# Kernel optimization log

Measured on AMD Instinct MI355X. Metric: run time of the kernel, lower is better.

The kernel has to match this reference:

```python
import jax, jax.numpy as jnp
from jax import lax
import numpy as np

B = 16
E, NH, FF, L = 768, 12, 3072, 8
D = E // NH  # 64, per-head dim
PATCH_DIM = 16 * 16 * 16  # 4096


def setup_inputs() -> dict:
    key = jax.random.key(0)
    ks = jax.random.split(key, 16)
    s = 0.02
    def n(k, shape):
        return jax.random.normal(k, shape, dtype=jnp.float32) * s
    return {
        "x": jax.random.normal(ks[0], (B, 512, 512, 3), dtype=jnp.float32),
        "conv1_w": n(ks[1], (3, 3, 3, 16)), "conv1_b": jnp.zeros((16,), jnp.float32),
        "conv2_w": n(ks[2], (3, 3, 16, 16)), "conv2_b": jnp.zeros((16,), jnp.float32),
        "proj_w": n(ks[3], (PATCH_DIM, E)), "proj_b": jnp.zeros((E,), jnp.float32),
        "Wq": n(ks[4], (L, E, E)), "bq": jnp.zeros((L, E), jnp.float32),
        "Wk": n(ks[5], (L, E, E)), "bk": jnp.zeros((L, E), jnp.float32),
        "Wv": n(ks[6], (L, E, E)), "bv": jnp.zeros((L, E), jnp.float32),
        "Wo": n(ks[7], (L, E, E)), "bo": jnp.zeros((L, E), jnp.float32),
        "W1": n(ks[8], (L, E, FF)), "b1": jnp.zeros((L, FF), jnp.float32),
        "W2": n(ks[9], (L, FF, E)), "b2": jnp.zeros((L, E), jnp.float32),
        "ln1_g": jnp.ones((L, E), jnp.float32), "ln1_b": jnp.zeros((L, E), jnp.float32),
        "ln2_g": jnp.ones((L, E), jnp.float32), "ln2_b": jnp.zeros((L, E), jnp.float32),
        "head_w": n(ks[10], (E, 1)), "head_b": jnp.zeros((1,), jnp.float32),
    }


def _ln(x, g, b, eps=1e-6):
    m = jnp.mean(x, axis=-1, keepdims=True)
    v = jnp.var(x, axis=-1, keepdims=True)
    return (x - m) * lax.rsqrt(v + eps) * g + b


def _forward(x, conv1_w, conv1_b, conv2_w, conv2_b, proj_w, proj_b,
             Wq, bq, Wk, bk, Wv, bv, Wo, bo, W1, b1, W2, b2,
             ln1_g, ln1_b, ln2_g, ln2_b, head_w, head_b):
    dn = ('NHWC', 'HWIO', 'NHWC')
    h = jax.nn.relu(lax.conv_general_dilated(x, conv1_w, (1, 1), 'VALID', dimension_numbers=dn) + conv1_b)
    h = lax.reduce_window(h, -jnp.inf, lax.max, (1, 2, 2, 1), (1, 2, 2, 1), 'VALID')  # (B,255,255,16)
    h = jax.nn.relu(lax.conv_general_dilated(h, conv2_w, (1, 1), 'VALID', dimension_numbers=dn) + conv2_b)
    h = lax.reduce_window(h, -jnp.inf, lax.max, (1, 2, 2, 1), (1, 2, 2, 1), 'VALID')  # (B,126,126,16)
    # tf.image.extract_patches 16x16 stride 16 SAME: pad 126 -> 128 (1 before, 1 after)
    h = jnp.pad(h, ((0, 0), (1, 1), (1, 1), (0, 0)))
    Bc = h.shape[0]
    patches = h.reshape(Bc, 8, 16, 8, 16, 16).transpose(0, 1, 3, 2, 4, 5).reshape(Bc, 64, PATCH_DIM)
    t = patches @ proj_w + proj_b  # (B,64,768)
    scale = 1.0 / jnp.sqrt(jnp.float32(D))  # tf code scales by sqrt(per-head key dim)
    for i in range(L):
        q = (t @ Wq[i] + bq[i]).reshape(Bc, -1, NH, D).transpose(0, 2, 1, 3)
        k = (t @ Wk[i] + bk[i]).reshape(Bc, -1, NH, D).transpose(0, 2, 1, 3)
        v = (t @ Wv[i] + bv[i]).reshape(Bc, -1, NH, D).transpose(0, 2, 1, 3)
        w = jax.nn.softmax(jnp.einsum('bhqd,bhkd->bhqk', q, k) * scale, axis=-1)
        a = jnp.einsum('bhqk,bhkd->bhqd', w, v)  # (B,H,S,D)
        # FAITHFUL to original: reshape (B,H,S,D) -> (B,S,E) directly (no transpose back)
        a = a.reshape(Bc, -1, E)
        a = a @ Wo[i] + bo[i]
        o1 = _ln(t + a, ln1_g[i], ln1_b[i])
        f = jax.nn.relu(o1 @ W1[i] + b1[i]) @ W2[i] + b2[i]
        t = _ln(o1 + f, ln2_g[i], ln2_b[i])
    pooled = jnp.mean(t, axis=1)  # GlobalAveragePooling1D
    return jax.nn.sigmoid(pooled @ head_w + head_b)


def reference(x, conv1_w, conv1_b, conv2_w, conv2_b, proj_w, proj_b,
              Wq, bq, Wk, bk, Wv, bv, Wo, bo, W1, b1, W2, b2,
              ln1_g, ln1_b, ln2_g, ln2_b, head_w, head_b):
    return _forward(x, conv1_w, conv1_b, conv2_w, conv2_b, proj_w, proj_b,
                    Wq, bq, Wk, bk, Wv, bv, Wo, bo, W1, b1, W2, b2,
                    ln1_g, ln1_b, ln2_g, ln2_b, head_w, head_b)
```

## Files before the change

### kernel.cpp

```cpp
#include <hip/hip_runtime.h>
#include <hip/hip_bf16.h>
#include <cstdint>
#include <cstddef>

typedef __bf16 bf16;
typedef __attribute__((ext_vector_type(8))) __bf16 bf16x8;
typedef __attribute__((ext_vector_type(4))) float f32x4;

__global__ __launch_bounds__(256) void wtrans(const float* __restrict__ src,
    bf16* __restrict__ dst, int K, int N) {
  __shared__ float tile[32][33];
  int l = blockIdx.z;
  src += (size_t)l * K * N; dst += (size_t)l * K * N;
  int n0 = blockIdx.x * 32, k0 = blockIdx.y * 32;
  int tx = threadIdx.x & 31, ty = threadIdx.x >> 5;
#pragma unroll
  for (int i = 0; i < 4; i++) {
    int k = ty + i * 8;
    tile[k][tx] = src[(size_t)(k0 + k) * N + n0 + tx];
  }
  __syncthreads();
#pragma unroll
  for (int i = 0; i < 4; i++) {
    int n = ty + i * 8;
    dst[(size_t)(n0 + n) * K + k0 + tx] = (bf16)tile[tx][n];
  }
}

__global__ __launch_bounds__(256) void conv1_mfma(const float* __restrict__ x,
    const float* __restrict__ w, const float* __restrict__ bias,
    bf16* __restrict__ out) {
  __shared__ alignas(16) bf16 xs[34 * 35 * 8];
  int t = threadIdx.x;
  int bx = blockIdx.x, by = blockIdx.y, b = blockIdx.z;
  int r0 = 32 * by, c0 = 32 * bx;
  for (int i = t; i < 34 * 35; i += 256) {
    int rr = i / 35, cc = i % 35;
    int gr = min(r0 + rr, 511), gc = min(c0 + cc, 511);
    const float* ip = x + ((size_t)(b * 512 + gr) * 512 + gc) * 3;
    bf16x8 pv = {(bf16)ip[0], (bf16)ip[1], (bf16)ip[2],
                 (bf16)0.f, (bf16)0.f, (bf16)0.f, (bf16)0.f, (bf16)0.f};
    *(bf16x8*)&xs[i * 8] = pv;
  }
  int lane = t & 63, wave = t >> 6;
  int lr = lane & 15, lq = lane >> 4;
  bf16x8 bfrag[3];
#pragma unroll
  for (int ky = 0; ky < 3; ky++) {
    bf16x8 v;
#pragma unroll
    for (int j = 0; j < 8; j++)
      v[j] = (lq < 3 && j < 3) ? (bf16)w[((ky * 3 + lq) * 3 + j) * 16 + lr] : (bf16)0.f;
    bfrag[ky] = v;
  }
  float bco = bias[lr];
  __syncthreads();
#pragma unroll
  for (int yy = 0; yy < 4; yy++) {
    int Y = wave * 4 + yy;
    int yp = by * 16 + Y;
    int cy = 2 * Y;
#pragma unroll
    for (int hx = 0; hx < 2; hx++) {
      f32x4 a0 = {0.f, 0.f, 0.f, 0.f}, a1 = {0.f, 0.f, 0.f, 0.f};
      int pbase = hx * 16 + lr + lq;
#pragma unroll
      for (int ky = 0; ky < 3; ky++) {
        bf16x8 f0 = *(const bf16x8*)&xs[((cy + ky) * 35 + pbase) * 8];
        a0 = __builtin_amdgcn_mfma_f32_16x16x32_bf16(f0, bfrag[ky], a0, 0, 0, 0);
      }
#pragma unroll
      for (int ky = 0; ky < 3; ky++) {
        bf16x8 f1 = *(const bf16x8*)&xs[((cy + 1 + ky) * 35 + pbase) * 8];
        a1 = __builtin_amdgcn_mfma_f32_16x16x32_bf16(f1, bfrag[ky], a1, 0, 0, 0);
      }
      float m0 = fmaxf(fmaxf(a0[0], a0[1]), fmaxf(a1[0], a1[1]));
      float m1 = fmaxf(fmaxf(a0[2], a0[3]), fmaxf(a1[2], a1[3]));
      m0 = fmaxf(m0 + bco, 0.f);
      m1 = fmaxf(m1 + bco, 0.f);
      int xp0 = bx * 16 + hx * 8 + 2 * lq, xp1 = xp0 + 1;
      if (yp < 255) {
        bf16* op = out + ((size_t)(b * 255 + yp) * 255) * 16 + lr;
        if (xp0 < 255) op[xp0 * 16] = (bf16)m0;
        if (xp1 < 255) op[xp1 * 16] = (bf16)m1;
      }
    }
  }
}

__global__ __launch_bounds__(256) void conv2_mfma(const bf16* __restrict__ in,
    const float* __restrict__ w, const float* __restrict__ bias,
    bf16* __restrict__ patches) {
  __shared__ alignas(16) bf16 xlo[1156 * 8];
  __shared__ alignas(16) bf16 xhi[1156 * 8];
  __shared__ float ws[2304];
  int t = threadIdx.x;
  int tx = blockIdx.x, ty = blockIdx.y, b = blockIdx.z;
  for (int i = t; i < 2304; i += 256) ws[i] = w[i];
  int r0 = 32 * ty - 2, c0 = 32 * tx - 2;
  for (int i = t; i < 1156; i += 256) {
    int rr = i / 34, cc = i % 34;
    int gr = min(max(r0 + rr, 0), 254), gc = min(max(c0 + cc, 0), 254);
    const bf16* ip = in + ((size_t)(b * 255 + gr) * 255 + gc) * 16;
    *(uint4*)&xlo[i * 8] = *(const uint4*)ip;
    *(uint4*)&xhi[i * 8] = *(const uint4*)(ip + 8);
  }
  __syncthreads();
  int lane = t & 63, wave = t >> 6;
  int lr = lane & 15, lq = lane >> 4;
  int tapsel = lq >> 1;
  int ci0 = (lq & 1) * 8;
  bf16x8 bfrag[5];
  int koff[5];
#pragma unroll
  for (int c2 = 0; c2 < 5; c2++) {
    int tap = 2 * c2 + tapsel;
    bf16x8 v;
#pragma unroll
    for (int j = 0; j < 8; j++)
      v[j] = (tap < 9) ? (bf16)ws[tap * 256 + (ci0 + j) * 16 + lr] : (bf16)0.f;
    bfrag[c2] = v;
    int tc = min(tap, 8);
    koff[c2] = (tc / 3) * 34 + (tc % 3);
  }
  const bf16* plane = (lq & 1) ? xhi : xlo;
  float bco = bias[lr];
  bf16* pout = patches + ((size_t)(b * 64 + ty * 8 + tx) * 4096);
#pragma unroll
  for (int yy = 0; yy < 4; yy++) {
    int Y = wave * 4 + yy;
    int yp = ty * 16 + Y;
    bool padrow = (yp == 0 || yp == 127);
#pragma unroll
    for (int hx = 0; hx < 2; hx++) {
      f32x4 a0 = {0.f, 0.f, 0.f, 0.f}, a1 = {0.f, 0.f, 0.f, 0.f};
      int base0 = (2 * Y) * 34 + hx * 16 + lr;
      int base1 = base0 + 34;
#pragma unroll
      for (int c2 = 0; c2 < 5; c2++) {
        bf16x8 f0 = *(const bf16x8*)&plane[(base0 + koff[c2]) * 8];
        a0 = __builtin_amdgcn_mfma_f32_16x16x32_bf16(f0, bfrag[c2], a0, 0, 0, 0);
      }
#pragma unroll
      for (int c2 = 0; c2 < 5; c2++) {
        bf16x8 f1 = *(const bf16x8*)&plane[(base1 + koff[c2]) * 8];
        a1 = __builtin_amdgcn_mfma_f32_16x16x32_bf16(f1, bfrag[c2], a1, 0, 0, 0);
      }
      float m0 = fmaxf(fmaxf(a0[0], a0[1]), fmaxf(a1[0], a1[1]));
      float m1 = fmaxf(fmaxf(a0[2], a0[3]), fmaxf(a1[2], a1[3]));
      m0 = fmaxf(m0 + bco, 0.f);
      m1 = fmaxf(m1 + bco, 0.f);
      int px0 = hx * 8 + 2 * lq, px1 = px0 + 1;
      int xp0 = tx * 16 + px0, xp1 = xp0 + 1;
      if (padrow || xp0 == 0) m0 = 0.f;
      if (padrow || xp1 == 127) m1 = 0.f;
      pout[Y * 256 + px0 * 16 + lr] = (bf16)m0;
      pout[Y * 256 + px1 * 16 + lr] = (bf16)m1;
    }
  }
}

#define LSTR 72

template<int MODE>
__device__ __forceinline__ void gemm_core(const bf16* __restrict__ A,
    const bf16* __restrict__ Bt, const float* __restrict__ bias,
    float* __restrict__ Cf, bf16* __restrict__ Cb,
    int bm, int bn, int N, int K, int k0, int kc) {
  __shared__ alignas(16) bf16 As[64 * LSTR];
  __shared__ alignas(16) bf16 Bs[64 * LSTR];
  int t = threadIdx.x, lane = t & 63, wave = t >> 6;
  int wm = (wave >> 1) * 32, wn = (wave & 1) * 32;
  int lq = lane >> 4, lr = lane & 15;
  f32x4 acc[2][2];
#pragma unroll
  for (int i = 0; i < 2; i++)
#pragma unroll
  for (int j = 0; j < 2; j++) acc[i][j] = (f32x4){0.f, 0.f, 0.f, 0.f};
  int r = t >> 2, c = (t & 3) * 16;
  const bf16* Ap = A + (size_t)(bm + r) * K + k0 + c;
  const bf16* Bp = Bt + (size_t)(bn + r) * K + k0 + c;
  bf16* AsW = &As[r * LSTR + c];
  bf16* BsW = &Bs[r * LSTR + c];
  uint4 a0 = *(const uint4*)Ap, a1 = *(const uint4*)(Ap + 8);
  uint4 b0 = *(const uint4*)Bp, b1 = *(const uint4*)(Bp + 8);
  for (int kk = 64; kk <= kc; kk += 64) {
    *(uint4*)AsW = a0; *(uint4*)(AsW + 8) = a1;
    *(uint4*)BsW = b0; *(uint4*)(BsW + 8) = b1;
    __syncthreads();
    if (kk < kc) {
      Ap += 64; Bp += 64;
      a0 = *(const uint4*)Ap; a1 = *(const uint4*)(Ap + 8);
      b0 = *(const uint4*)Bp; b1 = *(const uint4*)(Bp + 8);
    }
#pragma unroll
    for (int ks = 0; ks < 2; ks++) {
      bf16x8 af0 = *(const bf16x8*)&As[(wm + lr) * LSTR + ks * 32 + lq * 8];
      bf16x8 af1 = *(const bf16x8*)&As[(wm + 16 + lr) * LSTR + ks * 32 + lq * 8];
      bf16x8 bfr0 = *(const bf16x8*)&Bs[(wn + lr) * LSTR + ks * 32 + lq * 8];
      bf16x8 bfr1 = *(const bf16x8*)&Bs[(wn + 16 + lr) * LSTR + ks * 32 + lq * 8];
      acc[0][0] = __builtin_amdgcn_mfma_f32_16x16x32_bf16(af0, bfr0, acc[0][0], 0, 0, 0);
      acc[0][1] = __builtin_amdgcn_mfma_f32_16x16x32_bf16(af0, bfr1, acc[0][1], 0, 0, 0);
      acc[1][0] = __builtin_amdgcn_mfma_f32_16x16x32_bf16(af1, bfr0, acc[1][0], 0, 0, 0);
      acc[1][1] = __builtin_amdgcn_mfma_f32_16x16x32_bf16(af1, bfr1, acc[1][1], 0, 0, 0);
    }
    __syncthreads();
  }
#pragma unroll
  for (int mi = 0; mi < 2; mi++)
#pragma unroll
  for (int ni = 0; ni < 2; ni++) {
    int col = bn + wn + ni * 16 + lr;
#pragma unroll
    for (int rr = 0; rr < 4; rr++) {
      int row = bm + wm + mi * 16 + lq * 4 + rr;
      float v = acc[mi][ni][rr];
      if (MODE == 1) {
        v = fmaxf(v + bias[col], 0.f);
        Cb[(size_t)row * N + col] = (bf16)v;
      } else {
        Cf[(size_t)row * N + col] = v;
      }
    }
  }
}

template<int MODE>
__global__ __launch_bounds__(256) void gemm_std(const bf16* __restrict__ A,
    const bf16* __restrict__ Bt, const float* __restrict__ bias,
    float* __restrict__ Cf, bf16* __restrict__ Cb, int N, int K, int KC) {
  int s = blockIdx.z;
  float* Cfp = Cf ? Cf + (size_t)s * 1024 * N : nullptr;
  gemm_core<MODE>(A, Bt, bias, Cfp, Cb, blockIdx.y * 64, blockIdx.x * 64, N, K, s * KC, KC);
}

__global__ __launch_bounds__(256) void gemm_qkv(const bf16* __restrict__ A,
    const bf16* __restrict__ Btq, const bf16* __restrict__ Btk, const bf16* __restrict__ Btv,
    float* __restrict__ qp, float* __restrict__ kp, float* __restrict__ vp) {
  int z = blockIdx.z;
  int sel = z >> 1, s = z & 1;
  const bf16* Bt = (sel == 0) ? Btq : (sel == 1) ? Btk : Btv;
  float* C = ((sel == 0) ? qp : (sel == 1) ? kp : vp) + (size_t)s * 786432;
  gemm_core<0>(A, Bt, nullptr, C, nullptr, blockIdx.y * 64, blockIdx.x * 64, 768, 768, s * 384, 384);
}

__global__ __launch_bounds__(256) void attn_kernel(const float* __restrict__ Qp,
    const float* __restrict__ Kp, const float* __restrict__ Vp,
    const float* __restrict__ bq, const float* __restrict__ bk, const float* __restrict__ bv,
    bf16* __restrict__ Aout) {
  __shared__ alignas(16) bf16 qs[64 * 72];
  __shared__ alignas(16) bf16 ks[64 * 72];
  __shared__ alignas(16) bf16 vt[64 * 72];
  __shared__ alignas(16) bf16 ps[64 * 72];
  int t = threadIdx.x;
  int bh = blockIdx.x; int b = bh / 12, h = bh % 12;
  size_t base = (size_t)b * 49152 + h * 64;
  const float* qb0 = Qp + base; const float* qb1 = qb0 + 786432;
  const float* kb0 = Kp + base; const float* kb1 = kb0 + 786432;
  const float* vb0 = Vp + base; const float* vb1 = vb0 + 786432;
  {
    int s = t >> 2, d0 = (t & 3) * 16;
    alignas(16) bf16 qv[16], kv[16];
#pragma unroll
    for (int j = 0; j < 16; j += 4) {
      float4 q0 = *(const float4*)(qb0 + (size_t)s * 768 + d0 + j);
      float4 q1 = *(const float4*)(qb1 + (size_t)s * 768 + d0 + j);
      float4 qb4 = *(const float4*)(bq + h * 64 + d0 + j);
      float4 k0 = *(const float4*)(kb0 + (size_t)s * 768 + d0 + j);
      float4 k1 = *(const float4*)(kb1 + (size_t)s * 768 + d0 + j);
      float4 kb4 = *(const float4*)(bk + h * 64 + d0 + j);
      qv[j + 0] = (bf16)(q0.x + q1.x + qb4.x);
      qv[j + 1] = (bf16)(q0.y + q1.y + qb4.y);
      qv[j + 2] = (bf16)(q0.z + q1.z + qb4.z);
      qv[j + 3] = (bf16)(q0.w + q1.w + qb4.w);
      kv[j + 0] = (bf16)(k0.x + k1.x + kb4.x);
      kv[j + 1] = (bf16)(k0.y + k1.y + kb4.y);
      kv[j + 2] = (bf16)(k0.z + k1.z + kb4.z);
      kv[j + 3] = (bf16)(k0.w + k1.w + kb4.w);
    }
    *(uint4*)&qs[s * 72 + d0] = *(uint4*)&qv[0];
    *(uint4*)&qs[s * 72 + d0 + 8] = *(uint4*)&qv[8];
    *(uint4*)&ks[s * 72 + d0] = *(uint4*)&kv[0];
    *(uint4*)&ks[s * 72 + d0 + 8] = *(uint4*)&kv[8];
    int d = t & 63, s0 = (t >> 6) * 16;
    float bvd = bv[h * 64 + d];
    alignas(16) bf16 vv[16];
#pragma unroll
    for (int i = 0; i < 16; i++)
      vv[i] = (bf16)(vb0[(size_t)(s0 + i) * 768 + d] + vb1[(size_t)(s0 + i) * 768 + d] + bvd);
    *(uint4*)&vt[d * 72 + s0] = *(uint4*)&vv[0];
    *(uint4*)&vt[d * 72 + s0 + 8] = *(uint4*)&vv[8];
  }
  __syncthreads();
  int lane = t & 63, wave = t >> 6;
  int lr = lane & 15, lq = lane >> 4;
  int r0 = wave * 16;
  f32x4 sc[4];
#pragma unroll
  for (int j = 0; j < 4; j++) sc[j] = (f32x4){0.f, 0.f, 0.f, 0.f};
#pragma unroll
  for (int kslice = 0; kslice < 2; kslice++) {
    bf16x8 a = *(const bf16x8*)&qs[(r0 + lr) * 72 + kslice * 32 + lq * 8];
#pragma unroll
    for (int nj = 0; nj < 4; nj++) {
      bf16x8 bb = *(const bf16x8*)&ks[(nj * 16 + lr) * 72 + kslice * 32 + lq * 8];
      sc[nj] = __builtin_amdgcn_mfma_f32_16x16x32_bf16(a, bb, sc[nj], 0, 0, 0);
    }
  }
#pragma unroll
  for (int nj = 0; nj < 4; nj++)
#pragma unroll
  for (int rr = 0; rr < 4; rr++) sc[nj][rr] *= 0.125f;
  float pw[4][4];
#pragma unroll
  for (int rr = 0; rr < 4; rr++) {
    float m = fmaxf(fmaxf(sc[0][rr], sc[1][rr]), fmaxf(sc[2][rr], sc[3][rr]));
#pragma unroll
    for (int off = 1; off < 16; off <<= 1) m = fmaxf(m, __shfl_xor(m, off));
    float e0 = __expf(sc[0][rr] - m), e1 = __expf(sc[1][rr] - m);
    float e2 = __expf(sc[2][rr] - m), e3 = __expf(sc[3][rr] - m);
    float sm = e0 + e1 + e2 + e3;
#pragma unroll
    for (int off = 1; off < 16; off <<= 1) sm += __shfl_xor(sm, off);
    float inv = 1.f / sm;
    pw[0][rr] = e0 * inv; pw[1][rr] = e1 * inv;
    pw[2][rr] = e2 * inv; pw[3][rr] = e3 * inv;
  }
#pragma unroll
  for (int nj = 0; nj < 4; nj++)
#pragma unroll
  for (int rr = 0; rr < 4; rr++)
    ps[(r0 + lq * 4 + rr) * 72 + nj * 16 + lr] = (bf16)pw[nj][rr];
  __syncthreads();
  f32x4 oc[4];
#pragma unroll
  for (int j = 0; j < 4; j++) oc[j] = (f32x4){0.f, 0.f, 0.f, 0.f};
#pragma unroll
  for (int kslice = 0; kslice < 2; kslice++) {
    bf16x8 a = *(const bf16x8*)&ps[(r0 + lr) * 72 + kslice * 32 + lq * 8];
#pragma unroll
    for (int nj = 0; nj < 4; nj++) {
      bf16x8 bb = *(const bf16x8*)&vt[(nj * 16 + lr) * 72 + kslice * 32 + lq * 8];
      oc[nj] = __builtin_amdgcn_mfma_f32_16x16x32_bf16(a, bb, oc[nj], 0, 0, 0);
    }
  }
  bf16* ob = Aout + (size_t)b * 49152 + h * 4096;
#pragma unroll
  for (int nj = 0; nj < 4; nj++)
#pragma unroll
  for (int rr = 0; rr < 4; rr++)
    ob[(r0 + lq * 4 + rr) * 64 + nj * 16 + lr] = (bf16)oc[nj][rr];
}

template<int S>
__global__ __launch_bounds__(256) void ln_kernel(const float* __restrict__ X,
    const float* __restrict__ Y, const float* __restrict__ yb,
    const float* __restrict__ g, const float* __restrict__ bta,
    float* __restrict__ Of, bf16* __restrict__ Ob) {
  int row = blockIdx.x, t = threadIdx.x;
  const float* xp = X + (size_t)row * 768;
  float vals[3]; float s = 0.f, s2 = 0.f;
#pragma unroll
  for (int i = 0; i < 3; i++) {
    int e = t + 256 * i;
    float v = xp[e] + yb[e];
#pragma unroll
    for (int p = 0; p < S; p++) v += Y[(size_t)p * 786432 + (size_t)row * 768 + e];
    vals[i] = v; s += v; s2 = fmaf(v, v, s2);
  }
#pragma unroll
  for (int off = 32; off > 0; off >>= 1) { s += __shfl_xor(s, off); s2 += __shfl_xor(s2, off); }
  __shared__ float rs[4], rs2[4];
  if ((t & 63) == 0) { rs[t >> 6] = s; rs2[t >> 6] = s2; }
  __syncthreads();
  s = rs[0] + rs[1] + rs[2] + rs[3];
  s2 = rs2[0] + rs2[1] + rs2[2] + rs2[3];
  float mean = s * (1.f / 768.f);
  float var = s2 * (1.f / 768.f) - mean * mean;
  float rstd = rsqrtf(var + 1e-6f);
  float* ofp = Of + (size_t)row * 768;
  bf16* obp = Ob + (size_t)row * 768;
#pragma unroll
  for (int i = 0; i < 3; i++) {
    int e = t + 256 * i;
    float o = (vals[i] - mean) * rstd * g[e] + bta[e];
    ofp[e] = o; obp[e] = (bf16)o;
  }
}

__global__ __launch_bounds__(256) void reduce2(const float* __restrict__ P,
    const float* __restrict__ bias, float* __restrict__ Of, bf16* __restrict__ Ob) {
  int row = blockIdx.x, t = threadIdx.x;
#pragma unroll
  for (int i = 0; i < 3; i++) {
    int e = t + 256 * i;
    float v = P[(size_t)row * 768 + e] + P[786432 + (size_t)row * 768 + e] + bias[e];
    Of[(size_t)row * 768 + e] = v;
    Ob[(size_t)row * 768 + e] = (bf16)v;
  }
}

__global__ __launch_bounds__(256) void head_kernel(const float* __restrict__ T,
    const float* __restrict__ hw, const float* __restrict__ hbp, float* __restrict__ out) {
  int b = blockIdx.x, t = threadIdx.x;
  float acc = 0.f;
#pragma unroll
  for (int i = 0; i < 3; i++) {
    int e = t + 256 * i;
    float s = 0.f;
    for (int si = 0; si < 64; si++) s += T[(size_t)(b * 64 + si) * 768 + e];
    acc = fmaf(s * (1.f / 64.f), hw[e], acc);
  }
#pragma unroll
  for (int off = 32; off > 0; off >>= 1) acc += __shfl_xor(acc, off);
  __shared__ float rs[4];
  if ((t & 63) == 0) rs[t >> 6] = acc;
  __syncthreads();
  if (t == 0) {
    float z = rs[0] + rs[1] + rs[2] + rs[3] + hbp[0];
    out[b] = 1.f / (1.f + expf(-z));
  }
}

extern "C" void kernel_launch(void* const* d_in, const int* in_sizes, int n_in,
                              void* d_out, int out_size, void* d_ws, size_t ws_size,
                              hipStream_t stream) {
  const float* x     = (const float*)d_in[0];
  const float* c1w   = (const float*)d_in[1];
  const float* c1b   = (const float*)d_in[2];
  const float* c2w   = (const float*)d_in[3];
  const float* c2b   = (const float*)d_in[4];
  const float* projw = (const float*)d_in[5];
  const float* projb = (const float*)d_in[6];
  const float* Wq    = (const float*)d_in[7];
  const float* bq    = (const float*)d_in[8];
  const float* Wk    = (const float*)d_in[9];
  const float* bk    = (const float*)d_in[10];
  const float* Wv    = (const float*)d_in[11];
  const float* bv    = (const float*)d_in[12];
  const float* Wo    = (const float*)d_in[13];
  const float* bo    = (const float*)d_in[14];
  const float* W1    = (const float*)d_in[15];
  const float* b1    = (const float*)d_in[16];
  const float* W2    = (const float*)d_in[17];
  const float* b2    = (const float*)d_in[18];
  const float* ln1g  = (const float*)d_in[19];
  const float* ln1b  = (const float*)d_in[20];
  const float* ln2g  = (const float*)d_in[21];
  const float* ln2b  = (const float*)d_in[22];
  const float* headw = (const float*)d_in[23];
  const float* headb = (const float*)d_in[24];
  float* out = (float*)d_out;

  char* wp = (char*)d_ws;
  auto alloc = [&](size_t bytes) { char* p = wp; wp += (bytes + 255) & ~(size_t)255; return p; };
  bf16* c1p     = (bf16*)alloc((size_t)16 * 255 * 255 * 16 * 2);
  bf16* patches = (bf16*)alloc((size_t)1024 * 4096 * 2);
  bf16* projT   = (bf16*)alloc((size_t)4096 * 768 * 2);
  bf16* WqT     = (bf16*)alloc((size_t)8 * 768 * 768 * 2);
  bf16* WkT     = (bf16*)alloc((size_t)8 * 768 * 768 * 2);
  bf16* WvT     = (bf16*)alloc((size_t)8 * 768 * 768 * 2);
  bf16* WoT     = (bf16*)alloc((size_t)8 * 768 * 768 * 2);
  bf16* W1T     = (bf16*)alloc((size_t)8 * 768 * 3072 * 2);
  bf16* W2T     = (bf16*)alloc((size_t)8 * 3072 * 768 * 2);
  float* pp     = (float*)alloc((size_t)2 * 1024 * 768 * 4);
  float* tf     = (float*)alloc((size_t)1024 * 768 * 4);
  bf16*  tb     = (bf16*)alloc((size_t)1024 * 768 * 2);
  float* qp     = (float*)alloc((size_t)2 * 1024 * 768 * 4);
  float* kp     = (float*)alloc((size_t)2 * 1024 * 768 * 4);
  float* vp     = (float*)alloc((size_t)2 * 1024 * 768 * 4);
  float* wop    = (float*)alloc((size_t)2 * 1024 * 768 * 4);
  float* w2p    = (float*)alloc((size_t)4 * 1024 * 768 * 4);
  bf16*  ab     = (bf16*)alloc((size_t)1024 * 768 * 2);
  float* o1f    = (float*)alloc((size_t)1024 * 768 * 4);
  bf16*  o1b    = (bf16*)alloc((size_t)1024 * 768 * 2);
  bf16*  hbuf   = (bf16*)alloc((size_t)1024 * 3072 * 2);

  wtrans<<<dim3(24, 128, 1), 256, 0, stream>>>(projw, projT, 4096, 768);
  wtrans<<<dim3(24, 24, 8), 256, 0, stream>>>(Wq, WqT, 768, 768);
  wtrans<<<dim3(24, 24, 8), 256, 0, stream>>>(Wk, WkT, 768, 768);
  wtrans<<<dim3(24, 24, 8), 256, 0, stream>>>(Wv, WvT, 768, 768);
  wtrans<<<dim3(24, 24, 8), 256, 0, stream>>>(Wo, WoT, 768, 768);
  wtrans<<<dim3(96, 24, 8), 256, 0, stream>>>(W1, W1T, 768, 3072);
  wtrans<<<dim3(24, 96, 8), 256, 0, stream>>>(W2, W2T, 3072, 768);

  conv1_mfma<<<dim3(16, 16, 16), 256, 0, stream>>>(x, c1w, c1b, c1p);
  conv2_mfma<<<dim3(8, 8, 16), 256, 0, stream>>>(c1p, c2w, c2b, patches);
  gemm_std<0><<<dim3(12, 16, 2), 256, 0, stream>>>(patches, projT, nullptr, pp, nullptr, 768, 4096, 2048);
  reduce2<<<1024, 256, 0, stream>>>(pp, projb, tf, tb);

  for (int i = 0; i < 8; i++) {
    gemm_qkv<<<dim3(12, 16, 6), 256, 0, stream>>>(tb,
        WqT + (size_t)i * 589824, WkT + (size_t)i * 589824, WvT + (size_t)i * 589824,
        qp, kp, vp);
    attn_kernel<<<192, 256, 0, stream>>>(qp, kp, vp,
        bq + i * 768, bk + i * 768, bv + i * 768, ab);
    gemm_std<0><<<dim3(12, 16, 2), 256, 0, stream>>>(ab, WoT + (size_t)i * 589824,
        nullptr, wop, nullptr, 768, 768, 384);
    ln_kernel<2><<<1024, 256, 0, stream>>>(tf, wop, bo + i * 768,
        ln1g + i * 768, ln1b + i * 768, o1f, o1b);
    gemm_std<1><<<dim3(48, 16, 1), 256, 0, stream>>>(o1b, W1T + (size_t)i * 2359296,
        b1 + i * 3072, nullptr, hbuf, 3072, 768, 768);
    gemm_std<0><<<dim3(12, 16, 4), 256, 0, stream>>>(hbuf, W2T + (size_t)i * 2359296,
        nullptr, w2p, nullptr, 768, 3072, 768);
    ln_kernel<4><<<1024, 256, 0, stream>>>(o1f, w2p, b2 + i * 768,
        ln2g + i * 768, ln2b + i * 768, tf, tb);
  }
  head_kernel<<<16, 256, 0, stream>>>(tf, headw, headb, out);
}
```

Baseline: 910.4 us.

## Enlarge GEMM block tile to 128x128 with 4x4 MFMA per wave

The shared GEMM core moves from 64x64 to 128x128 output tiles. Each wave now computes a 64x64 sub-tile using 16 accumulators. The shared-memory loader is restructured so half the threads stage A rows and half stage B rows, and launch bounds ask for two blocks per CU. All GEMM grids shrink by a factor of four. The aim is more data reuse per LDS load, at the risk of too few blocks to fill the GPU and higher register pressure.

```diff
diff --git a/kernel.cpp b/kernel.cpp
--- a/kernel.cpp
+++ b/kernel.cpp
@@ -167,49 +167,55 @@
     const bf16* __restrict__ Bt, const float* __restrict__ bias,
     float* __restrict__ Cf, bf16* __restrict__ Cb,
     int bm, int bn, int N, int K, int k0, int kc) {
-  __shared__ alignas(16) bf16 As[64 * LSTR];
-  __shared__ alignas(16) bf16 Bs[64 * LSTR];
+  __shared__ alignas(16) bf16 As[128 * LSTR];
+  __shared__ alignas(16) bf16 Bs[128 * LSTR];
   int t = threadIdx.x, lane = t & 63, wave = t >> 6;
-  int wm = (wave >> 1) * 32, wn = (wave & 1) * 32;
+  int wm = (wave >> 1) * 64, wn = (wave & 1) * 64;
   int lq = lane >> 4, lr = lane & 15;
-  f32x4 acc[2][2];
-#pragma unroll
-  for (int i = 0; i < 2; i++)
-#pragma unroll
-  for (int j = 0; j < 2; j++) acc[i][j] = (f32x4){0.f, 0.f, 0.f, 0.f};
-  int r = t >> 2, c = (t & 3) * 16;
-  const bf16* Ap = A + (size_t)(bm + r) * K + k0 + c;
-  const bf16* Bp = Bt + (size_t)(bn + r) * K + k0 + c;
-  bf16* AsW = &As[r * LSTR + c];
-  bf16* BsW = &Bs[r * LSTR + c];
-  uint4 a0 = *(const uint4*)Ap, a1 = *(const uint4*)(Ap + 8);
-  uint4 b0 = *(const uint4*)Bp, b1 = *(const uint4*)(Bp + 8);
+  f32x4 acc[4][4];
+#pragma unroll
+  for (int i = 0; i < 4; i++)
+#pragma unroll
+  for (int j = 0; j < 4; j++) acc[i][j] = (f32x4){0.f, 0.f, 0.f, 0.f};
+  int srow = t & 127;
+  const bf16* Gp = ((t >> 7) ? Bt + (size_t)(bn + srow) * K
+                             : A + (size_t)(bm + srow) * K) + k0;
+  bf16* Ls = ((t >> 7) ? Bs : As) + srow * LSTR;
+  uint4 st[4], su[4];
+#pragma unroll
+  for (int i = 0; i < 4; i++) { st[i] = *(const uint4*)(Gp + i * 16);
+                                su[i] = *(const uint4*)(Gp + i * 16 + 8); }
   for (int kk = 64; kk <= kc; kk += 64) {
-    *(uint4*)AsW = a0; *(uint4*)(AsW + 8) = a1;
-    *(uint4*)BsW = b0; *(uint4*)(BsW + 8) = b1;
+#pragma unroll
+    for (int i = 0; i < 4; i++) { *(uint4*)(Ls + i * 16) = st[i];
+                                  *(uint4*)(Ls + i * 16 + 8) = su[i]; }
     __syncthreads();
     if (kk < kc) {
-      Ap += 64; Bp += 64;
-      a0 = *(const uint4*)Ap; a1 = *(const uint4*)(Ap + 8);
-      b0 = *(const uint4*)Bp; b1 = *(const uint4*)(Bp + 8);
+      Gp += 64;
+#pragma unroll
+      for (int i = 0; i < 4; i++) { st[i] = *(const uint4*)(Gp + i * 16);
+                                    su[i] = *(const uint4*)(Gp + i * 16 + 8); }
     }
 #pragma unroll
     for (int ks = 0; ks < 2; ks++) {
-      bf16x8 af0 = *(const bf16x8*)&As[(wm + lr) * LSTR + ks * 32 + lq * 8];
-      bf16x8 af1 = *(const bf16x8*)&As[(wm + 16 + lr) * LSTR + ks * 32 + lq * 8];
-      bf16x8 bfr0 = *(const bf16x8*)&Bs[(wn + lr) * LSTR + ks * 32 + lq * 8];
-      bf16x8 bfr1 = *(const bf16x8*)&Bs[(wn + 16 + lr) * LSTR + ks * 32 + lq * 8];
-      acc[0][0] = __builtin_amdgcn_mfma_f32_16x16x32_bf16(af0, bfr0, acc[0][0], 0, 0, 0);
-      acc[0][1] = __builtin_amdgcn_mfma_f32_16x16x32_bf16(af0, bfr1, acc[0][1], 0, 0, 0);
-      acc[1][0] = __builtin_amdgcn_mfma_f32_16x16x32_bf16(af1, bfr0, acc[1][0], 0, 0, 0);
-      acc[1][1] = __builtin_amdgcn_mfma_f32_16x16x32_bf16(af1, bfr1, acc[1][1], 0, 0, 0);
+      bf16x8 af[4], bfr[4];
+#pragma unroll
+      for (int i = 0; i < 4; i++) {
+        af[i]  = *(const bf16x8*)&As[(wm + i * 16 + lr) * LSTR + ks * 32 + lq * 8];
+        bfr[i] = *(const bf16x8*)&Bs[(wn + i * 16 + lr) * LSTR + ks * 32 + lq * 8];
+      }
+#pragma unroll
+      for (int mi = 0; mi < 4; mi++)
+#pragma unroll
+      for (int ni = 0; ni < 4; ni++)
+        acc[mi][ni] = __builtin_amdgcn_mfma_f32_16x16x32_bf16(af[mi], bfr[ni], acc[mi][ni], 0, 0, 0);
     }
     __syncthreads();
   }
 #pragma unroll
-  for (int mi = 0; mi < 2; mi++)
-#pragma unroll
-  for (int ni = 0; ni < 2; ni++) {
+  for (int mi = 0; mi < 4; mi++)
+#pragma unroll
+  for (int ni = 0; ni < 4; ni++) {
     int col = bn + wn + ni * 16 + lr;
 #pragma unroll
     for (int rr = 0; rr < 4; rr++) {
@@ -226,22 +232,22 @@
 }
 
 template<int MODE>
-__global__ __launch_bounds__(256) void gemm_std(const bf16* __restrict__ A,
+__global__ __launch_bounds__(256, 2) void gemm_std(const bf16* __restrict__ A,
     const bf16* __restrict__ Bt, const float* __restrict__ bias,
     float* __restrict__ Cf, bf16* __restrict__ Cb, int N, int K, int KC) {
   int s = blockIdx.z;
   float* Cfp = Cf ? Cf + (size_t)s * 1024 * N : nullptr;
-  gemm_core<MODE>(A, Bt, bias, Cfp, Cb, blockIdx.y * 64, blockIdx.x * 64, N, K, s * KC, KC);
-}
-
-__global__ __launch_bounds__(256) void gemm_qkv(const bf16* __restrict__ A,
+  gemm_core<MODE>(A, Bt, bias, Cfp, Cb, blockIdx.y * 128, blockIdx.x * 128, N, K, s * KC, KC);
+}
+
+__global__ __launch_bounds__(256, 2) void gemm_qkv(const bf16* __restrict__ A,
     const bf16* __restrict__ Btq, const bf16* __restrict__ Btk, const bf16* __restrict__ Btv,
     float* __restrict__ qp, float* __restrict__ kp, float* __restrict__ vp) {
   int z = blockIdx.z;
   int sel = z >> 1, s = z & 1;
   const bf16* Bt = (sel == 0) ? Btq : (sel == 1) ? Btk : Btv;
   float* C = ((sel == 0) ? qp : (sel == 1) ? kp : vp) + (size_t)s * 786432;
-  gemm_core<0>(A, Bt, nullptr, C, nullptr, blockIdx.y * 64, blockIdx.x * 64, 768, 768, s * 384, 384);
+  gemm_core<0>(A, Bt, nullptr, C, nullptr, blockIdx.y * 128, blockIdx.x * 128, 768, 768, s * 384, 384);
 }
 
 __global__ __launch_bounds__(256) void attn_kernel(const float* __restrict__ Qp,
@@ -486,22 +492,22 @@
 
   conv1_mfma<<<dim3(16, 16, 16), 256, 0, stream>>>(x, c1w, c1b, c1p);
   conv2_mfma<<<dim3(8, 8, 16), 256, 0, stream>>>(c1p, c2w, c2b, patches);
-  gemm_std<0><<<dim3(12, 16, 2), 256, 0, stream>>>(patches, projT, nullptr, pp, nullptr, 768, 4096, 2048);
+  gemm_std<0><<<dim3(6, 8, 2), 256, 0, stream>>>(patches, projT, nullptr, pp, nullptr, 768, 4096, 2048);
   reduce2<<<1024, 256, 0, stream>>>(pp, projb, tf, tb);
 
   for (int i = 0; i < 8; i++) {
-    gemm_qkv<<<dim3(12, 16, 6), 256, 0, stream>>>(tb,
+    gemm_qkv<<<dim3(6, 8, 6), 256, 0, stream>>>(tb,
         WqT + (size_t)i * 589824, WkT + (size_t)i * 589824, WvT + (size_t)i * 589824,
         qp, kp, vp);
     attn_kernel<<<192, 256, 0, stream>>>(qp, kp, vp,
         bq + i * 768, bk + i * 768, bv + i * 768, ab);
-    gemm_std<0><<<dim3(12, 16, 2), 256, 0, stream>>>(ab, WoT + (size_t)i * 589824,
+    gemm_std<0><<<dim3(6, 8, 2), 256, 0, stream>>>(ab, WoT + (size_t)i * 589824,
         nullptr, wop, nullptr, 768, 768, 384);
     ln_kernel<2><<<1024, 256, 0, stream>>>(tf, wop, bo + i * 768,
         ln1g + i * 768, ln1b + i * 768, o1f, o1b);
-    gemm_std<1><<<dim3(48, 16, 1), 256, 0, stream>>>(o1b, W1T + (size_t)i * 2359296,
+    gemm_std<1><<<dim3(24, 8, 1), 256, 0, stream>>>(o1b, W1T + (size_t)i * 2359296,
         b1 + i * 3072, nullptr, hbuf, 3072, 768, 768);
-    gemm_std<0><<<dim3(12, 16, 4), 256, 0, stream>>>(hbuf, W2T + (size_t)i * 2359296,
+    gemm_std<0><<<dim3(6, 8, 4), 256, 0, stream>>>(hbuf, W2T + (size_t)i * 2359296,
         nullptr, w2p, nullptr, 768, 3072, 768);
     ln_kernel<4><<<1024, 256, 0, stream>>>(o1f, w2p, b2 + i * 768,
         ln2g + i * 768, ln2b + i * 768, tf, tb);
```

Result: slower. 1.786 ms (+96.2%).
